# Kernel optimization log

Hardware: AMD Instinct MI355X
Metric: run time of the kernel (lower is better)

Reference implementation:

```python
import jax, jax.numpy as jnp
import numpy as np

EPS = 1e-5

def _mish(v):
    return v * jnp.tanh(jax.nn.softplus(v))

def _ln(v):
    m = jnp.mean(v, axis=-1, keepdims=True)
    var = jnp.var(v, axis=-1, keepdims=True)
    return (v - m) * jax.lax.rsqrt(var + EPS)

def setup_inputs() -> dict:
    B, S, D, H_HID = 1024, 64, 768, 3072
    key = jax.random.key(0)
    ks = jax.random.split(key, 12)
    s = 0.02  # init scale for weights
    return {
        "x": jax.random.normal(ks[0], (B, S, D), dtype=jnp.float32),
        "c": jax.random.normal(ks[1], (B, D), dtype=jnp.float32),
        "W_mod": jax.random.normal(ks[2], (D, 6 * D), dtype=jnp.float32) * s,
        "b_mod": jax.random.normal(ks[3], (6 * D,), dtype=jnp.float32) * s,
        "W_qkv": jax.random.normal(ks[4], (D, 3 * D), dtype=jnp.float32) * s,
        "b_qkv": jax.random.normal(ks[5], (3 * D,), dtype=jnp.float32) * s,
        "W_out": jax.random.normal(ks[6], (D, D), dtype=jnp.float32) * s,
        "b_out": jax.random.normal(ks[7], (D,), dtype=jnp.float32) * s,
        "W_f1": jax.random.normal(ks[8], (D, H_HID), dtype=jnp.float32) * s,
        "b_f1": jax.random.normal(ks[9], (H_HID,), dtype=jnp.float32) * s,
        "W_f2": jax.random.normal(ks[10], (H_HID, D), dtype=jnp.float32) * s,
        "b_f2": jax.random.normal(ks[11], (D,), dtype=jnp.float32) * s,
    }

def reference(x, c, W_mod, b_mod, W_qkv, b_qkv, W_out, b_out, W_f1, b_f1, W_f2, b_f2):
    B, S, D = x.shape
    num_heads = 12
    head_dim = D // num_heads

    # AdaLN modulation: Mish(c) -> linear -> 6 vectors, broadcast over S
    mod = _mish(c) @ W_mod + b_mod              # [B, 6D]
    mod = mod[:, None, :]                       # [B, 1, 6D]
    shift1, scale1, gate1, shift2, scale2, gate2 = jnp.split(mod, 6, axis=-1)

    # --- attention sub-block ---
    h = _ln(x) * (1.0 + scale1) + shift1        # [B, S, D]
    qkv = (h @ W_qkv + b_qkv).reshape(B, S, 3, num_heads, head_dim)
    q = qkv[:, :, 0].transpose(0, 2, 1, 3)      # [B, H, S, hd]
    k = qkv[:, :, 1].transpose(0, 2, 1, 3)
    v = qkv[:, :, 2].transpose(0, 2, 1, 3)
    attn = jnp.einsum("bhsd,bhtd->bhst", q, k) * (head_dim ** -0.5)
    attn = jax.nn.softmax(attn, axis=-1)
    h = jnp.einsum("bhst,bhtd->bhsd", attn, v)  # [B, H, S, hd]
    h = h.transpose(0, 2, 1, 3).reshape(B, S, D)
    h = h @ W_out + b_out
    x = x + gate1 * h

    # --- FFN sub-block ---
    h = _ln(x) * (1.0 + scale2) + shift2
    h = _mish(h @ W_f1 + b_f1) @ W_f2 + b_f2
    x = x + gate2 * h
    return x
```

## Files before the change

### kernel.cpp

```cpp
#include <hip/hip_runtime.h>

typedef unsigned int uint;
typedef unsigned short ushort;

using bf16x8 = __attribute__((ext_vector_type(8))) short;
using f32x4  = __attribute__((ext_vector_type(4))) float;

#define LOAD16(g, l) __builtin_amdgcn_global_load_lds( \
    (const __attribute__((address_space(1))) void*)(g), \
    (__attribute__((address_space(3))) void*)(l), 16, 0, 0)

__device__ __forceinline__ ushort f2b(float f){
  uint u = __float_as_uint(f);
  u = (u + 0x7FFFu + ((u >> 16) & 1u)) >> 16;
  return (ushort)u;
}
__device__ __forceinline__ float b2f(ushort h){
  return __uint_as_float(((uint)h) << 16);
}
__device__ __forceinline__ float mishf(float v){
  float t = __expf(v);
  float u = t * (t + 2.f);
  float r = u * __builtin_amdgcn_rcpf(u + 2.f);
  return v > 15.f ? v : v * r;
}

__global__ __launch_bounds__(256) void transpose_f32_bf16(
    const float* __restrict__ W, ushort* __restrict__ Wt, int K, int N)
{
  __shared__ float tile[32][33];
  int k0 = blockIdx.x * 32, n0 = blockIdx.y * 32;
  int tx = threadIdx.x & 31, ty = threadIdx.x >> 5;
  #pragma unroll
  for (int r = ty; r < 32; r += 8)
    tile[r][tx] = W[(size_t)(k0 + r) * N + n0 + tx];
  __syncthreads();
  #pragma unroll
  for (int r = ty; r < 32; r += 8)
    Wt[(size_t)(n0 + r) * K + k0 + tx] = f2b(tile[tx][r]);
}

__global__ void mish_to_bf16(const float* __restrict__ in, ushort* __restrict__ out, int n){
  int i = blockIdx.x * blockDim.x + threadIdx.x;
  int stride = gridDim.x * blockDim.x;
  for (; i < n; i += stride) out[i] = f2b(mishf(in[i]));
}

__global__ __launch_bounds__(256) void ln_modulate(
    const float* __restrict__ xin,
    const float* __restrict__ modb,
    ushort* __restrict__ out,
    int shift_off, int scale_off)
{
  int row = blockIdx.x;
  int t = threadIdx.x;
  const float* xr = xin + (size_t)row * 768;
  float v0 = xr[t], v1 = xr[t + 256], v2 = xr[t + 512];
  float s  = v0 + v1 + v2;
  float ss = v0*v0 + v1*v1 + v2*v2;
  #pragma unroll
  for (int off = 32; off > 0; off >>= 1){
    s  += __shfl_down(s, off);
    ss += __shfl_down(ss, off);
  }
  __shared__ float rs[4], rss[4];
  int wave = t >> 6, lane = t & 63;
  if (lane == 0){ rs[wave] = s; rss[wave] = ss; }
  __syncthreads();
  s  = rs[0] + rs[1] + rs[2] + rs[3];
  ss = rss[0] + rss[1] + rss[2] + rss[3];
  float mean = s * (1.f / 768.f);
  float var  = ss * (1.f / 768.f) - mean * mean;
  float rstd = rsqrtf(var + 1e-5f);
  const float* mr = modb + (size_t)(row >> 6) * 4608;
  ushort* orow = out + (size_t)row * 768;
  #pragma unroll
  for (int e = 0; e < 3; e++){
    int n = t + e * 256;
    float xv = (e == 0 ? v0 : (e == 1 ? v1 : v2));
    float sc = 1.f + mr[scale_off + n];
    float sh = mr[shift_off + n];
    orow[n] = f2b((xv - mean) * rstd * sc + sh);
  }
}

template<int MODE>
__global__ __launch_bounds__(256) void gemm_bt(
    const ushort* __restrict__ A,
    const ushort* __restrict__ Bt,
    const float* __restrict__ bias,
    float* __restrict__ out_f,
    ushort* __restrict__ out_h,
    const float* __restrict__ resid,
    const float* __restrict__ gate,
    int M, int N, int K)
{
  __shared__ ushort sA[2][128 * 32];
  __shared__ ushort sB[2][128 * 32];
  int tid  = threadIdx.x;
  int lane = tid & 63, wave = tid >> 6;
  int l15  = lane & 15, quad = lane >> 4;
  int m0 = blockIdx.x * 128, n0 = blockIdx.y * 128;
  int wm = (wave & 1) * 64, wn = (wave >> 1) * 64;

  int r0  = wave * 32 + (lane >> 2);
  int r1  = r0 + 16;
  int cs  = lane & 3;
  int kc0 = cs ^ ((r0 >> 1) & 3);
  int kc1 = cs ^ ((r1 >> 1) & 3);
  const ushort* gA0 = A  + (size_t)(m0 + r0) * K + kc0 * 8;
  const ushort* gA1 = A  + (size_t)(m0 + r1) * K + kc1 * 8;
  const ushort* gB0 = Bt + (size_t)(n0 + r0) * K + kc0 * 8;
  const ushort* gB1 = Bt + (size_t)(n0 + r1) * K + kc1 * 8;
  int wofs = wave * 1024;

  int sw = quad ^ ((l15 >> 1) & 3);
  int ra = (wm + l15) * 32 + sw * 8;
  int rb = (wn + l15) * 32 + sw * 8;

  f32x4 acc[4][4];
  #pragma unroll
  for (int i = 0; i < 4; i++)
    #pragma unroll
    for (int j = 0; j < 4; j++) acc[i][j] = (f32x4){0.f, 0.f, 0.f, 0.f};

  int nk = K >> 5;

  LOAD16(gA0, &sA[0][wofs]);
  LOAD16(gA1, &sA[0][wofs + 512]);
  LOAD16(gB0, &sB[0][wofs]);
  LOAD16(gB1, &sB[0][wofs + 512]);
  gA0 += 32; gA1 += 32; gB0 += 32; gB1 += 32;
  __syncthreads();

  for (int kt = 0; kt < nk - 1; kt++){
    int cur = kt & 1, nxt = cur ^ 1;
    LOAD16(gA0, &sA[nxt][wofs]);
    LOAD16(gA1, &sA[nxt][wofs + 512]);
    LOAD16(gB0, &sB[nxt][wofs]);
    LOAD16(gB1, &sB[nxt][wofs + 512]);
    gA0 += 32; gA1 += 32; gB0 += 32; gB1 += 32;

    bf16x8 af[4], bv[4];
    #pragma unroll
    for (int i = 0; i < 4; i++) af[i] = *(const bf16x8*)(&sA[cur][ra + i * 512]);
    #pragma unroll
    for (int j = 0; j < 4; j++) bv[j] = *(const bf16x8*)(&sB[cur][rb + j * 512]);
    #pragma unroll
    for (int i = 0; i < 4; i++)
      #pragma unroll
      for (int j = 0; j < 4; j++)
        acc[i][j] = __builtin_amdgcn_mfma_f32_16x16x32_bf16(af[i], bv[j], acc[i][j], 0, 0, 0);

    __syncthreads();
  }

  {
    int cur = (nk - 1) & 1;
    bf16x8 af[4], bv[4];
    #pragma unroll
    for (int i = 0; i < 4; i++) af[i] = *(const bf16x8*)(&sA[cur][ra + i * 512]);
    #pragma unroll
    for (int j = 0; j < 4; j++) bv[j] = *(const bf16x8*)(&sB[cur][rb + j * 512]);
    #pragma unroll
    for (int i = 0; i < 4; i++)
      #pragma unroll
      for (int j = 0; j < 4; j++)
        acc[i][j] = __builtin_amdgcn_mfma_f32_16x16x32_bf16(af[i], bv[j], acc[i][j], 0, 0, 0);
  }

  float bias_v[4];
  #pragma unroll
  for (int j = 0; j < 4; j++) bias_v[j] = bias[n0 + wn + j * 16 + l15];
  #pragma unroll
  for (int i = 0; i < 4; i++){
    int mb = m0 + wm + i * 16 + quad * 4;
    #pragma unroll
    for (int j = 0; j < 4; j++){
      int n = n0 + wn + j * 16 + l15;
      #pragma unroll
      for (int r = 0; r < 4; r++){
        int m = mb + r;
        float v = acc[i][j][r] + bias_v[j];
        size_t idx = (size_t)m * N + n;
        if (MODE == 0)      out_f[idx] = v;
        else if (MODE == 1) out_h[idx] = f2b(v);
        else if (MODE == 2){
          float g = gate[(size_t)(m >> 6) * 4608 + n];
          out_f[idx] = resid[idx] + g * v;
        } else              out_h[idx] = f2b(mishf(v));
      }
    }
  }
}

__global__ __launch_bounds__(256) void attn64(
    const ushort* __restrict__ qkv,
    ushort* __restrict__ out)
{
  __shared__ float kk[64][68];
  __shared__ float vv[64][68];
  __shared__ float sc[64][65];
  __shared__ float red[2][4][64];
  int bi = blockIdx.x, h = blockIdx.y;
  int t  = threadIdx.x;
  int s4 = t >> 2, p = t & 3;
  size_t rowbase = ((size_t)bi * 64 + s4) * 2304 + h * 64;

  {
    const uint4* kp = (const uint4*)(qkv + rowbase + 768  + p * 16);
    const uint4* vp = (const uint4*)(qkv + rowbase + 1536 + p * 16);
    union { uint4 u; ushort s[8]; } k0, k1, v0, v1;
    k0.u = kp[0]; k1.u = kp[1]; v0.u = vp[0]; v1.u = vp[1];
    #pragma unroll
    for (int e = 0; e < 8; e++){
      kk[s4][p * 16 + e]     = b2f(k0.s[e]);
      kk[s4][p * 16 + 8 + e] = b2f(k1.s[e]);
      vv[s4][p * 16 + e]     = b2f(v0.s[e]);
      vv[s4][p * 16 + 8 + e] = b2f(v1.s[e]);
    }
  }
  float qr[64];
  {
    const uint4* qp = (const uint4*)(qkv + rowbase);
    #pragma unroll
    for (int c = 0; c < 8; c++){
      union { uint4 u; ushort s[8]; } q; q.u = qp[c];
      #pragma unroll
      for (int e = 0; e < 8; e++) qr[c * 8 + e] = b2f(q.s[e]);
    }
  }
  __syncthreads();

  float scr[16]; float mx = -1e30f;
  #pragma unroll
  for (int jj = 0; jj < 16; jj++){
    int j = p * 16 + jj;
    float a = 0.f;
    #pragma unroll
    for (int d = 0; d < 64; d++) a += qr[d] * kk[j][d];
    a *= 0.125f;
    scr[jj] = a; mx = fmaxf(mx, a);
  }
  red[0][p][s4] = mx;
  __syncthreads();
  float rmx = fmaxf(fmaxf(red[0][0][s4], red[0][1][s4]),
                    fmaxf(red[0][2][s4], red[0][3][s4]));
  float sm = 0.f;
  #pragma unroll
  for (int jj = 0; jj < 16; jj++){
    float e = __expf(scr[jj] - rmx);
    sm += e;
    sc[s4][p * 16 + jj] = e;
  }
  red[1][p][s4] = sm;
  __syncthreads();
  float rinv = 1.f / (red[1][0][s4] + red[1][1][s4] + red[1][2][s4] + red[1][3][s4]);

  float o[16];
  #pragma unroll
  for (int e = 0; e < 16; e++) o[e] = 0.f;
  for (int j = 0; j < 64; j++){
    float pj = sc[s4][j];
    #pragma unroll
    for (int e = 0; e < 16; e++) o[e] += pj * vv[j][p * 16 + e];
  }
  ushort* op = out + ((size_t)bi * 64 + s4) * 768 + h * 64 + p * 16;
  #pragma unroll
  for (int e = 0; e < 16; e++) op[e] = f2b(o[e] * rinv);
}

extern "C" void kernel_launch(void* const* d_in, const int* in_sizes, int n_in,
                              void* d_out, int out_size, void* d_ws, size_t ws_size,
                              hipStream_t stream)
{
  (void)in_sizes; (void)n_in; (void)out_size; (void)ws_size;
  const float* x     = (const float*)d_in[0];
  const float* c     = (const float*)d_in[1];
  const float* W_mod = (const float*)d_in[2];
  const float* b_mod = (const float*)d_in[3];
  const float* W_qkv = (const float*)d_in[4];
  const float* b_qkv = (const float*)d_in[5];
  const float* W_out = (const float*)d_in[6];
  const float* b_out = (const float*)d_in[7];
  const float* W_f1  = (const float*)d_in[8];
  const float* b_f1  = (const float*)d_in[9];
  const float* W_f2  = (const float*)d_in[10];
  const float* b_f2  = (const float*)d_in[11];
  float* out = (float*)d_out;

  char* ws = (char*)d_ws;
  size_t off = 0;
  auto alloc = [&](size_t bytes)->char* {
    char* p = ws + off; off += (bytes + 255) & ~(size_t)255; return p;
  };
  ushort* Wb_mod = (ushort*)alloc((size_t)768 * 4608 * 2);
  ushort* Wb_qkv = (ushort*)alloc((size_t)768 * 2304 * 2);
  ushort* Wb_out = (ushort*)alloc((size_t)768 * 768  * 2);
  ushort* Wb_f1  = (ushort*)alloc((size_t)768 * 3072 * 2);
  ushort* Wb_f2  = (ushort*)alloc((size_t)3072 * 768 * 2);
  ushort* c_act  = (ushort*)alloc((size_t)1024 * 768 * 2);
  float*  mod    = (float*) alloc((size_t)1024 * 4608 * 4);
  ushort* bufH   = (ushort*)alloc((size_t)16384 * 768  * 2);
  ushort* bufQKV = (ushort*)alloc((size_t)16384 * 2304 * 2);
  ushort* bufG   = (ushort*)alloc((size_t)16384 * 3072 * 2);

  transpose_f32_bf16<<<dim3(24, 144), 256, 0, stream>>>(W_mod, Wb_mod, 768, 4608);
  transpose_f32_bf16<<<dim3(24, 72),  256, 0, stream>>>(W_qkv, Wb_qkv, 768, 2304);
  transpose_f32_bf16<<<dim3(24, 24),  256, 0, stream>>>(W_out, Wb_out, 768, 768);
  transpose_f32_bf16<<<dim3(24, 96),  256, 0, stream>>>(W_f1,  Wb_f1,  768, 3072);
  transpose_f32_bf16<<<dim3(96, 24),  256, 0, stream>>>(W_f2,  Wb_f2,  3072, 768);
  mish_to_bf16<<<512, 256, 0, stream>>>(c, c_act, 1024 * 768);
  gemm_bt<0><<<dim3(8, 36), 256, 0, stream>>>(c_act, Wb_mod, b_mod, mod, nullptr,
                                              nullptr, nullptr, 1024, 4608, 768);

  for (int ch = 0; ch < 4; ch++){
    int b0 = ch * 256;
    const float* xc   = x   + (size_t)b0 * 64 * 768;
    float*       oc   = out + (size_t)b0 * 64 * 768;
    const float* modc = mod + (size_t)b0 * 4608;

    ln_modulate<<<16384, 256, 0, stream>>>(xc, modc, bufH, 0, 768);
    gemm_bt<1><<<dim3(128, 18), 256, 0, stream>>>(bufH, Wb_qkv, b_qkv, nullptr, bufQKV,
                                                  nullptr, nullptr, 16384, 2304, 768);
    attn64<<<dim3(256, 12), 256, 0, stream>>>(bufQKV, bufH);
    gemm_bt<2><<<dim3(128, 6), 256, 0, stream>>>(bufH, Wb_out, b_out, oc, nullptr,
                                                 xc, modc + 1536, 16384, 768, 768);
    ln_modulate<<<16384, 256, 0, stream>>>(oc, modc, bufH, 2304, 3072);
    gemm_bt<3><<<dim3(128, 24), 256, 0, stream>>>(bufH, Wb_f1, b_f1, nullptr, bufG,
                                                  nullptr, nullptr, 16384, 3072, 768);
    gemm_bt<2><<<dim3(128, 6), 256, 0, stream>>>(bufG, Wb_f2, b_f2, oc, nullptr,
                                                 oc, modc + 3840, 16384, 768, 3072);
  }
}
```

Measured before the change: 2.426 ms.

## Add 256x256-tile GEMM with 4-stage LDS pipeline for main projections

Adds a new gemm256 kernel that uses 256x256 output tiles, 8 waves, and a 4-buffer LDS ring with explicit vmcnt waits, so global loads are prefetched three K-slabs ahead. MFMA bursts are wrapped in setprio to favour math issue. The QKV, out-projection and FFN GEMMs now launch this kernel in place of the smaller-tile gemm_bt. The larger tiles raise reuse per load and cut global traffic, at the cost of 128KB of LDS per block, high register pressure, and fewer blocks (192 for N=768), which may underfill the GPU.

```diff
diff --git a/kernel.cpp b/kernel.cpp
--- a/kernel.cpp
+++ b/kernel.cpp
@@ -125,7 +125,6 @@
     for (int j = 0; j < 4; j++) acc[i][j] = (f32x4){0.f, 0.f, 0.f, 0.f};
 
   int nk = K >> 5;
-
   LOAD16(gA0, &sA[0][wofs]);
   LOAD16(gA1, &sA[0][wofs + 512]);
   LOAD16(gB0, &sB[0][wofs]);
@@ -182,6 +181,132 @@
       for (int r = 0; r < 4; r++){
         int m = mb + r;
         float v = acc[i][j][r] + bias_v[j];
+        size_t idx = (size_t)m * N + n;
+        if (MODE == 0)      out_f[idx] = v;
+        else if (MODE == 1) out_h[idx] = f2b(v);
+        else if (MODE == 2){
+          float g = gate[(size_t)(m >> 6) * 4608 + n];
+          out_f[idx] = resid[idx] + g * v;
+        } else              out_h[idx] = f2b(mishf(v));
+      }
+    }
+  }
+}
+
+template<int MODE>
+__global__ __launch_bounds__(512, 2) void gemm256(
+    const ushort* __restrict__ A,
+    const ushort* __restrict__ Bt,
+    const float* __restrict__ bias,
+    float* __restrict__ out_f,
+    ushort* __restrict__ out_h,
+    const float* __restrict__ resid,
+    const float* __restrict__ gate,
+    int M, int N, int K)
+{
+  __shared__ __align__(16) ushort sA[4 * 8192];
+  __shared__ __align__(16) ushort sB[4 * 8192];
+  int tid  = threadIdx.x;
+  int lane = tid & 63, wave = tid >> 6;
+  int l15  = lane & 15, quad = lane >> 4;
+  int m0 = blockIdx.x * 256, n0 = blockIdx.y * 256;
+  int wrow = wave & 1, wcol = wave >> 1;
+
+  int r  = tid >> 2;
+  int cs = tid & 3;
+  int kc = cs ^ ((r >> 1) & 3);
+  const ushort* gA0 = A  + (size_t)(m0 + r) * K + kc * 8;
+  const ushort* gA1 = A  + (size_t)(m0 + r + 128) * K + kc * 8;
+  const ushort* gB0 = Bt + (size_t)(n0 + r) * K + kc * 8;
+  const ushort* gB1 = Bt + (size_t)(n0 + r + 128) * K + kc * 8;
+  int wofs = wave * 512;
+
+  int sw = quad ^ ((l15 >> 1) & 3);
+  int ra = (wrow * 128 + l15) * 32 + sw * 8;
+  int rb = (wcol * 64  + l15) * 32 + sw * 8;
+
+  f32x4 acc[8][4];
+  #pragma unroll
+  for (int i = 0; i < 8; i++)
+    #pragma unroll
+    for (int j = 0; j < 4; j++) acc[i][j] = (f32x4){0.f, 0.f, 0.f, 0.f};
+
+  int nslab = K >> 5;
+
+  #pragma unroll
+  for (int s = 0; s < 3; s++){
+    int bo = s << 13;
+    int ko = s << 5;
+    LOAD16(gA0 + ko, &sA[bo + wofs]);
+    LOAD16(gA1 + ko, &sA[bo + wofs + 4096]);
+    LOAD16(gB0 + ko, &sB[bo + wofs]);
+    LOAD16(gB1 + ko, &sB[bo + wofs + 4096]);
+  }
+  asm volatile("s_waitcnt vmcnt(8)" ::: "memory");
+  __builtin_amdgcn_s_barrier();
+
+  #pragma unroll 1
+  for (int s = 0; s < nslab; s++){
+    int bo = (s & 3) << 13;
+    int bn = ((s + 3) & 3) << 13;
+    bool pf = (s + 3) < nslab;
+    int ko = (s + 3) << 5;
+    bf16x8 bv[4], af[4];
+
+    if (pf){
+      LOAD16(gA0 + ko, &sA[bn + wofs]);
+      LOAD16(gA1 + ko, &sA[bn + wofs + 4096]);
+    }
+    #pragma unroll
+    for (int j = 0; j < 4; j++) bv[j] = *(const bf16x8*)(&sB[bo + rb + j * 512]);
+    #pragma unroll
+    for (int i = 0; i < 4; i++) af[i] = *(const bf16x8*)(&sA[bo + ra + i * 512]);
+    __builtin_amdgcn_s_barrier();
+    asm volatile("s_waitcnt lgkmcnt(0)" ::: "memory");
+    __builtin_amdgcn_s_setprio(1);
+    #pragma unroll
+    for (int i = 0; i < 4; i++)
+      #pragma unroll
+      for (int j = 0; j < 4; j++)
+        acc[i][j] = __builtin_amdgcn_mfma_f32_16x16x32_bf16(af[i], bv[j], acc[i][j], 0, 0, 0);
+    __builtin_amdgcn_s_setprio(0);
+    __builtin_amdgcn_s_barrier();
+
+    if (pf){
+      LOAD16(gB0 + ko, &sB[bn + wofs]);
+      LOAD16(gB1 + ko, &sB[bn + wofs + 4096]);
+    }
+    #pragma unroll
+    for (int i = 0; i < 4; i++) af[i] = *(const bf16x8*)(&sA[bo + ra + 2048 + i * 512]);
+    __builtin_amdgcn_s_barrier();
+    asm volatile("s_waitcnt lgkmcnt(0)" ::: "memory");
+    __builtin_amdgcn_s_setprio(1);
+    #pragma unroll
+    for (int i = 0; i < 4; i++)
+      #pragma unroll
+      for (int j = 0; j < 4; j++)
+        acc[4 + i][j] = __builtin_amdgcn_mfma_f32_16x16x32_bf16(af[i], bv[j], acc[4 + i][j], 0, 0, 0);
+    __builtin_amdgcn_s_setprio(0);
+
+    if (s + 3 < nslab)      asm volatile("s_waitcnt vmcnt(8)" ::: "memory");
+    else if (s + 2 < nslab) asm volatile("s_waitcnt vmcnt(4)" ::: "memory");
+    else if (s + 1 < nslab) asm volatile("s_waitcnt vmcnt(0)" ::: "memory");
+    __builtin_amdgcn_s_barrier();
+  }
+
+  float bias_v[4];
+  #pragma unroll
+  for (int j = 0; j < 4; j++) bias_v[j] = bias[n0 + wcol * 64 + j * 16 + l15];
+  #pragma unroll
+  for (int i = 0; i < 8; i++){
+    int mb = m0 + wrow * 128 + i * 16 + quad * 4;
+    #pragma unroll
+    for (int j = 0; j < 4; j++){
+      int n = n0 + wcol * 64 + j * 16 + l15;
+      #pragma unroll
+      for (int rr = 0; rr < 4; rr++){
+        int m = mb + rr;
+        float v = acc[i][j][rr] + bias_v[j];
         size_t idx = (size_t)m * N + n;
         if (MODE == 0)      out_f[idx] = v;
         else if (MODE == 1) out_h[idx] = f2b(v);
@@ -321,15 +446,15 @@
     const float* modc = mod + (size_t)b0 * 4608;
 
     ln_modulate<<<16384, 256, 0, stream>>>(xc, modc, bufH, 0, 768);
-    gemm_bt<1><<<dim3(128, 18), 256, 0, stream>>>(bufH, Wb_qkv, b_qkv, nullptr, bufQKV,
-                                                  nullptr, nullptr, 16384, 2304, 768);
+    gemm256<1><<<dim3(64, 9), 512, 0, stream>>>(bufH, Wb_qkv, b_qkv, nullptr, bufQKV,
+                                                nullptr, nullptr, 16384, 2304, 768);
     attn64<<<dim3(256, 12), 256, 0, stream>>>(bufQKV, bufH);
-    gemm_bt<2><<<dim3(128, 6), 256, 0, stream>>>(bufH, Wb_out, b_out, oc, nullptr,
-                                                 xc, modc + 1536, 16384, 768, 768);
+    gemm256<2><<<dim3(64, 3), 512, 0, stream>>>(bufH, Wb_out, b_out, oc, nullptr,
+                                                xc, modc + 1536, 16384, 768, 768);
     ln_modulate<<<16384, 256, 0, stream>>>(oc, modc, bufH, 2304, 3072);
-    gemm_bt<3><<<dim3(128, 24), 256, 0, stream>>>(bufH, Wb_f1, b_f1, nullptr, bufG,
-                                                  nullptr, nullptr, 16384, 3072, 768);
-    gemm_bt<2><<<dim3(128, 6), 256, 0, stream>>>(bufG, Wb_f2, b_f2, oc, nullptr,
-                                                 oc, modc + 3840, 16384, 768, 3072);
-  }
-}
+    gemm256<3><<<dim3(64, 12), 512, 0, stream>>>(bufH, Wb_f1, b_f1, nullptr, bufG,
+                                                 nullptr, nullptr, 16384, 3072, 768);
+    gemm256<2><<<dim3(64, 3), 512, 0, stream>>>(bufG, Wb_f2, b_f2, oc, nullptr,
+                                                oc, modc + 3840, 16384, 768, 3072);
+  }
+}
```

Result: slower. 2.615 ms (+7.8%).
